# Kernel optimization log

Measured on AMD Instinct MI355X. Metric: run time of the kernel, lower is better.

Reference implementation:

```python
import jax, jax.numpy as jnp
import numpy as np

EPS = 1e-6

def _phi(x):
    # elu(x) + 1 feature map
    return jax.nn.elu(x) + 1.0

def setup_inputs() -> dict:
    key = jax.random.key(0)
    kq, kk, kv = jax.random.split(key, 3)
    N, L, S, H, D, M = 8, 4096, 4096, 8, 64, 64
    queries = jax.random.normal(kq, (N, L, H, D), dtype=jnp.float32)
    keys = jax.random.normal(kk, (N, S, H, D), dtype=jnp.float32)
    values = jax.random.normal(kv, (N, S, H, M), dtype=jnp.float32)
    key_mask = jnp.ones((N, S), dtype=jnp.float32)  # key_lengths.float_matrix
    return {"queries": queries, "keys": keys, "values": values, "key_mask": key_mask}

def reference(queries, keys, values, key_mask):
    Q = _phi(queries)                                   # [N,L,H,D]
    K = _phi(keys) * key_mask[:, :, None, None]         # [N,S,H,D]
    KV = jnp.einsum('nshd,nshm->nhmd', K, values)       # [N,H,M,D]
    Z = 1.0 / (jnp.einsum('nlhd,nhd->nlh', Q, K.sum(axis=1)) + EPS)  # [N,L,H]
    V = jnp.einsum('nlhd,nhmd,nlh->nlhm', Q, KV, Z)     # [N,L,H,M]
    return V
```

## Files before the change

kernel.cpp:

```cpp
#include <hip/hip_runtime.h>


#define SLEN 4096
#define LLEN 4096
#define NHTOT 64
#define HD   512
#define NSPLIT 16
#define EPSF 1e-6f

__device__ __forceinline__ float phi(float x) {
    return x > 0.0f ? x + 1.0f : __expf(x);
}

__device__ __forceinline__ void fma4(float4& a, float s, const float4& b) {
    a.x = fmaf(s, b.x, a.x);
    a.y = fmaf(s, b.y, a.y);
    a.z = fmaf(s, b.z, a.z);
    a.w = fmaf(s, b.w, a.w);
}

__global__ __launch_bounds__(256)
void la_phase1(const float* __restrict__ Kg, const float* __restrict__ Vg,
               const float* __restrict__ maskg,
               float* __restrict__ KVp, float* __restrict__ Ksump) {
    __shared__ float kb[64 * 68];
    __shared__ float vb[64 * 64];
    __shared__ float ksb[16 * 64];

    const int tid  = threadIdx.x;
    const int w    = tid >> 6;
    const int lane = tid & 63;
    const int nh   = blockIdx.y;
    const int n    = nh >> 3;
    const int h    = nh & 7;
    const int sp   = blockIdx.x;

    const int sr = tid >> 4;
    const int c4 = (tid & 15) * 4;
    const int wd = w & 1, wm = w >> 1;
    const int d0 = wd * 32 + (lane & 7) * 4;
    const int m0 = wm * 32 + (lane >> 3) * 4;

    const size_t base = (size_t)n * SLEN * HD + (size_t)h * 64;
    const float* mrow = maskg + (size_t)n * SLEN;
    const int sblock = sp * 256;

    float4 acc[4];
    #pragma unroll
    for (int i = 0; i < 4; ++i) acc[i] = make_float4(0.f, 0.f, 0.f, 0.f);
    float4 ksp = make_float4(0.f, 0.f, 0.f, 0.f);

    for (int t = 0; t < 4; ++t) {
        const int srow0 = sblock + t * 64;
        __syncthreads();
        #pragma unroll
        for (int u = 0; u < 4; ++u) {
            const int row = sr + u * 16;
            const int s   = srow0 + row;
            const size_t g = base + (size_t)s * HD + c4;
            float4 kf = *(const float4*)(Kg + g);
            const float mm = mrow[s];
            kf.x = phi(kf.x) * mm;
            kf.y = phi(kf.y) * mm;
            kf.z = phi(kf.z) * mm;
            kf.w = phi(kf.w) * mm;
            ksp.x += kf.x; ksp.y += kf.y; ksp.z += kf.z; ksp.w += kf.w;
            *(float4*)&kb[row * 68 + c4] = kf;
            *(float4*)&vb[row * 64 + c4] = *(const float4*)(Vg + g);
        }
        __syncthreads();
        #pragma unroll 8
        for (int s = 0; s < 64; ++s) {
            const float4 k4 = *(const float4*)&kb[s * 68 + d0];
            const float4 v4 = *(const float4*)&vb[s * 64 + m0];
            fma4(acc[0], k4.x, v4);
            fma4(acc[1], k4.y, v4);
            fma4(acc[2], k4.z, v4);
            fma4(acc[3], k4.w, v4);
        }
    }

    float* outp = KVp + ((size_t)sp * NHTOT + nh) * 4096;
    #pragma unroll
    for (int di = 0; di < 4; ++di)
        *(float4*)&outp[(d0 + di) * 64 + m0] = acc[di];

    *(float4*)&ksb[sr * 64 + c4] = ksp;
    __syncthreads();
    if (tid < 64) {
        float ssum = 0.f;
        #pragma unroll
        for (int r = 0; r < 16; ++r) ssum += ksb[r * 64 + tid];
        Ksump[((size_t)sp * NHTOT + nh) * 64 + tid] = ssum;
    }
}

__global__ __launch_bounds__(256)
void la_reduce(const float* __restrict__ KVp, const float* __restrict__ Ksump,
               float* __restrict__ KVt, float* __restrict__ Ksum) {
    const int nh  = blockIdx.x;
    const int tid = threadIdx.x;
    #pragma unroll
    for (int j = 0; j < 4; ++j) {
        const int f = (j * 256 + tid) * 4;
        float4 a = make_float4(0.f, 0.f, 0.f, 0.f);
        #pragma unroll
        for (int s = 0; s < NSPLIT; ++s) {
            const float4 v = *(const float4*)&KVp[((size_t)s * NHTOT + nh) * 4096 + f];
            a.x += v.x; a.y += v.y; a.z += v.z; a.w += v.w;
        }
        *(float4*)&KVt[(size_t)nh * 4096 + f] = a;
    }
    if (tid < 64) {
        float a = 0.f;
        #pragma unroll
        for (int s = 0; s < NSPLIT; ++s)
            a += Ksump[((size_t)s * NHTOT + nh) * 64 + tid];
        Ksum[nh * 64 + tid] = a;
    }
}

__global__ __launch_bounds__(256)
void la_phase2(const float* __restrict__ Qg, const float* __restrict__ KVt,
               const float* __restrict__ Ksum, float* __restrict__ Og) {
    __shared__ float Qs[128 * 68];
    __shared__ float KVs[64 * 64];
    __shared__ float KSs[64];

    const int tid = threadIdx.x;
    const int nh  = blockIdx.y;
    const int n   = nh >> 3;
    const int h   = nh & 7;
    const int lbase = blockIdx.x * 128;

    #pragma unroll
    for (int j = 0; j < 4; ++j) {
        const int f = (j * 256 + tid) * 4;
        *(float4*)&KVs[f] = *(const float4*)&KVt[(size_t)nh * 4096 + f];
    }
    if (tid < 16) *(float4*)&KSs[tid * 4] = *(const float4*)&Ksum[nh * 64 + tid * 4];

    const int sr = tid >> 4;
    const int c4 = (tid & 15) * 4;
    #pragma unroll
    for (int u = 0; u < 8; ++u) {
        const int row = sr + u * 16;
        float4 q = *(const float4*)&Qg[((size_t)(n * LLEN + lbase + row) * 8 + h) * 64 + c4];
        q.x = phi(q.x); q.y = phi(q.y); q.z = phi(q.z); q.w = phi(q.w);
        *(float4*)&Qs[row * 68 + c4] = q;
    }
    __syncthreads();

    const int w    = tid >> 6;
    const int lane = tid & 63;
    const int ty   = lane >> 4;
    const int tx   = lane & 15;
    const int m0   = tx * 4;
    const int rb   = w * 32 + ty;

    float4 acc[8];
    float  den[8];
    #pragma unroll
    for (int i = 0; i < 8; ++i) {
        acc[i] = make_float4(0.f, 0.f, 0.f, 0.f);
        den[i] = 0.f;
    }

    for (int d4 = 0; d4 < 16; ++d4) {
        const float4 ks = *(const float4*)&KSs[d4 * 4];
        float4 q4[8];
        #pragma unroll
        for (int i = 0; i < 8; ++i)
            q4[i] = *(const float4*)&Qs[(rb + 4 * i) * 68 + d4 * 4];
        #pragma unroll
        for (int i = 0; i < 8; ++i) {
            den[i] = fmaf(q4[i].x, ks.x, den[i]);
            den[i] = fmaf(q4[i].y, ks.y, den[i]);
            den[i] = fmaf(q4[i].z, ks.z, den[i]);
            den[i] = fmaf(q4[i].w, ks.w, den[i]);
        }
        #pragma unroll
        for (int dk = 0; dk < 4; ++dk) {
            const float4 kv = *(const float4*)&KVs[(d4 * 4 + dk) * 64 + m0];
            #pragma unroll
            for (int i = 0; i < 8; ++i)
                fma4(acc[i], (&q4[i].x)[dk], kv);
        }
    }

    #pragma unroll
    for (int i = 0; i < 8; ++i) {
        const int l = lbase + rb + 4 * i;
        const float z = 1.0f / (den[i] + EPSF);
        float4 o = acc[i];
        o.x *= z; o.y *= z; o.z *= z; o.w *= z;
        *(float4*)&Og[((size_t)(n * LLEN + l) * 8 + h) * 64 + m0] = o;
    }
}

extern "C" void kernel_launch(void* const* d_in, const int* in_sizes, int n_in,
                              void* d_out, int out_size, void* d_ws, size_t ws_size,
                              hipStream_t stream) {
    const float* Q    = (const float*)d_in[0];
    const float* K    = (const float*)d_in[1];
    const float* V    = (const float*)d_in[2];
    const float* mask = (const float*)d_in[3];
    float* out = (float*)d_out;

    float* KVp   = (float*)d_ws;
    float* Ksump = KVp + (size_t)NSPLIT * NHTOT * 4096;
    float* KVt   = Ksump + (size_t)NSPLIT * NHTOT * 64;
    float* Ksum  = KVt + (size_t)NHTOT * 4096;

    dim3 g1(NSPLIT, NHTOT);
    la_phase1<<<g1, 256, 0, stream>>>(K, V, mask, KVp, Ksump);

    la_reduce<<<NHTOT, 256, 0, stream>>>(KVp, Ksump, KVt, Ksum);

    dim3 g2(LLEN / 128, NHTOT);
    la_phase2<<<g2, 256, 0, stream>>>(Q, KVt, Ksum, out);
}
```

Baseline: 253.4 us.

## Give each wave its own KV tile in phase1 and enlarge phase2 row blocks

```diff
diff --git a/kernel.cpp b/kernel.cpp
--- a/kernel.cpp
+++ b/kernel.cpp
@@ -5,7 +5,7 @@
 #define LLEN 4096
 #define NHTOT 64
 #define HD   512
-#define NSPLIT 16
+#define NSPLIT 4
 #define EPSF 1e-6f
 
 __device__ __forceinline__ float phi(float x) {
@@ -23,8 +23,8 @@
 void la_phase1(const float* __restrict__ Kg, const float* __restrict__ Vg,
                const float* __restrict__ maskg,
                float* __restrict__ KVp, float* __restrict__ Ksump) {
-    __shared__ float kb[64 * 68];
-    __shared__ float vb[64 * 64];
+    __shared__ float kb[4][4096];
+    __shared__ float vb[4][4096];
     __shared__ float ksb[16 * 64];
 
     const int tid  = threadIdx.x;
@@ -35,58 +35,83 @@
     const int h    = nh & 7;
     const int sp   = blockIdx.x;
 
-    const int sr = tid >> 4;
-    const int c4 = (tid & 15) * 4;
-    const int wd = w & 1, wm = w >> 1;
-    const int d0 = wd * 32 + (lane & 7) * 4;
-    const int m0 = wm * 32 + (lane >> 3) * 4;
+    const int sr4 = lane >> 4;
+    const int c4  = (lane & 15) * 4;
+    const int d0  = (lane & 7) * 8;
+    const int m0  = (lane >> 3) * 8;
+
+    float* kw = kb[w];
+    float* vw = vb[w];
 
     const size_t base = (size_t)n * SLEN * HD + (size_t)h * 64;
     const float* mrow = maskg + (size_t)n * SLEN;
-    const int sblock = sp * 256;
-
-    float4 acc[4];
-    #pragma unroll
-    for (int i = 0; i < 4; ++i) acc[i] = make_float4(0.f, 0.f, 0.f, 0.f);
+
+    float4 acc[8][2];
+    #pragma unroll
+    for (int i = 0; i < 8; ++i) {
+        acc[i][0] = make_float4(0.f, 0.f, 0.f, 0.f);
+        acc[i][1] = make_float4(0.f, 0.f, 0.f, 0.f);
+    }
     float4 ksp = make_float4(0.f, 0.f, 0.f, 0.f);
 
     for (int t = 0; t < 4; ++t) {
-        const int srow0 = sblock + t * 64;
-        __syncthreads();
-        #pragma unroll
-        for (int u = 0; u < 4; ++u) {
-            const int row = sr + u * 16;
+        const int srow0 = sp * 1024 + t * 256 + w * 64;
+        #pragma unroll
+        for (int u = 0; u < 16; ++u) {
+            const int row = sr4 + u * 4;
             const int s   = srow0 + row;
             const size_t g = base + (size_t)s * HD + c4;
             float4 kf = *(const float4*)(Kg + g);
+            const float4 vf = *(const float4*)(Vg + g);
             const float mm = mrow[s];
             kf.x = phi(kf.x) * mm;
             kf.y = phi(kf.y) * mm;
             kf.z = phi(kf.z) * mm;
             kf.w = phi(kf.w) * mm;
             ksp.x += kf.x; ksp.y += kf.y; ksp.z += kf.z; ksp.w += kf.w;
-            *(float4*)&kb[row * 68 + c4] = kf;
-            *(float4*)&vb[row * 64 + c4] = *(const float4*)(Vg + g);
-        }
-        __syncthreads();
-        #pragma unroll 8
+            *(float4*)&kw[row * 64 + c4] = kf;
+            *(float4*)&vw[row * 64 + c4] = vf;
+        }
+        #pragma unroll 4
         for (int s = 0; s < 64; ++s) {
-            const float4 k4 = *(const float4*)&kb[s * 68 + d0];
-            const float4 v4 = *(const float4*)&vb[s * 64 + m0];
-            fma4(acc[0], k4.x, v4);
-            fma4(acc[1], k4.y, v4);
-            fma4(acc[2], k4.z, v4);
-            fma4(acc[3], k4.w, v4);
-        }
-    }
+            const float4 ka = *(const float4*)&kw[s * 64 + d0];
+            const float4 kz = *(const float4*)&kw[s * 64 + d0 + 4];
+            const float4 va = *(const float4*)&vw[s * 64 + m0];
+            const float4 vz = *(const float4*)&vw[s * 64 + m0 + 4];
+            fma4(acc[0][0], ka.x, va); fma4(acc[0][1], ka.x, vz);
+            fma4(acc[1][0], ka.y, va); fma4(acc[1][1], ka.y, vz);
+            fma4(acc[2][0], ka.z, va); fma4(acc[2][1], ka.z, vz);
+            fma4(acc[3][0], ka.w, va); fma4(acc[3][1], ka.w, vz);
+            fma4(acc[4][0], kz.x, va); fma4(acc[4][1], kz.x, vz);
+            fma4(acc[5][0], kz.y, va); fma4(acc[5][1], kz.y, vz);
+            fma4(acc[6][0], kz.z, va); fma4(acc[6][1], kz.z, vz);
+            fma4(acc[7][0], kz.w, va); fma4(acc[7][1], kz.w, vz);
+        }
+    }
+
+    *(float4*)&ksb[(w * 4 + sr4) * 64 + c4] = ksp;
+
+    #pragma unroll
+    for (int di = 0; di < 8; ++di) {
+        *(float4*)&kw[(d0 + di) * 64 + m0]     = acc[di][0];
+        *(float4*)&kw[(d0 + di) * 64 + m0 + 4] = acc[di][1];
+    }
+    __syncthreads();
 
     float* outp = KVp + ((size_t)sp * NHTOT + nh) * 4096;
     #pragma unroll
-    for (int di = 0; di < 4; ++di)
-        *(float4*)&outp[(d0 + di) * 64 + m0] = acc[di];
-
-    *(float4*)&ksb[sr * 64 + c4] = ksp;
-    __syncthreads();
+    for (int j = 0; j < 4; ++j) {
+        const int f = (j * 256 + tid) * 4;
+        float4 a  = *(const float4*)&kb[0][f];
+        const float4 b1 = *(const float4*)&kb[1][f];
+        const float4 b2 = *(const float4*)&kb[2][f];
+        const float4 b3 = *(const float4*)&kb[3][f];
+        a.x += b1.x + b2.x + b3.x;
+        a.y += b1.y + b2.y + b3.y;
+        a.z += b1.z + b2.z + b3.z;
+        a.w += b1.w + b2.w + b3.w;
+        *(float4*)&outp[f] = a;
+    }
     if (tid < 64) {
         float ssum = 0.f;
         #pragma unroll
@@ -120,10 +145,10 @@
     }
 }
 
-__global__ __launch_bounds__(256)
+__global__ __launch_bounds__(512)
 void la_phase2(const float* __restrict__ Qg, const float* __restrict__ KVt,
                const float* __restrict__ Ksum, float* __restrict__ Og) {
-    __shared__ float Qs[128 * 68];
+    __shared__ float Qs[512 * 68];
     __shared__ float KVs[64 * 64];
     __shared__ float KSs[64];
 
@@ -131,11 +156,11 @@
     const int nh  = blockIdx.y;
     const int n   = nh >> 3;
     const int h   = nh & 7;
-    const int lbase = blockIdx.x * 128;
-
-    #pragma unroll
-    for (int j = 0; j < 4; ++j) {
-        const int f = (j * 256 + tid) * 4;
+    const int lbase = blockIdx.x * 512;
+
+    #pragma unroll
+    for (int j = 0; j < 2; ++j) {
+        const int f = (j * 512 + tid) * 4;
         *(float4*)&KVs[f] = *(const float4*)&KVt[(size_t)nh * 4096 + f];
     }
     if (tid < 16) *(float4*)&KSs[tid * 4] = *(const float4*)&Ksum[nh * 64 + tid * 4];
@@ -143,8 +168,8 @@
     const int sr = tid >> 4;
     const int c4 = (tid & 15) * 4;
     #pragma unroll
-    for (int u = 0; u < 8; ++u) {
-        const int row = sr + u * 16;
+    for (int u = 0; u < 16; ++u) {
+        const int row = sr + u * 32;
         float4 q = *(const float4*)&Qg[((size_t)(n * LLEN + lbase + row) * 8 + h) * 64 + c4];
         q.x = phi(q.x); q.y = phi(q.y); q.z = phi(q.z); q.w = phi(q.w);
         *(float4*)&Qs[row * 68 + c4] = q;
@@ -156,24 +181,24 @@
     const int ty   = lane >> 4;
     const int tx   = lane & 15;
     const int m0   = tx * 4;
-    const int rb   = w * 32 + ty;
-
-    float4 acc[8];
-    float  den[8];
-    #pragma unroll
-    for (int i = 0; i < 8; ++i) {
+    const int rb   = w * 64 + ty;
+
+    float4 acc[16];
+    float  den[16];
+    #pragma unroll
+    for (int i = 0; i < 16; ++i) {
         acc[i] = make_float4(0.f, 0.f, 0.f, 0.f);
         den[i] = 0.f;
     }
 
     for (int d4 = 0; d4 < 16; ++d4) {
         const float4 ks = *(const float4*)&KSs[d4 * 4];
-        float4 q4[8];
-        #pragma unroll
-        for (int i = 0; i < 8; ++i)
+        float4 q4[16];
+        #pragma unroll
+        for (int i = 0; i < 16; ++i)
             q4[i] = *(const float4*)&Qs[(rb + 4 * i) * 68 + d4 * 4];
         #pragma unroll
-        for (int i = 0; i < 8; ++i) {
+        for (int i = 0; i < 16; ++i) {
             den[i] = fmaf(q4[i].x, ks.x, den[i]);
             den[i] = fmaf(q4[i].y, ks.y, den[i]);
             den[i] = fmaf(q4[i].z, ks.z, den[i]);
@@ -183,13 +208,13 @@
         for (int dk = 0; dk < 4; ++dk) {
             const float4 kv = *(const float4*)&KVs[(d4 * 4 + dk) * 64 + m0];
             #pragma unroll
-            for (int i = 0; i < 8; ++i)
+            for (int i = 0; i < 16; ++i)
                 fma4(acc[i], (&q4[i].x)[dk], kv);
         }
     }
 
     #pragma unroll
-    for (int i = 0; i < 8; ++i) {
+    for (int i = 0; i < 16; ++i) {
         const int l = lbase + rb + 4 * i;
         const float z = 1.0f / (den[i] + EPSF);
         float4 o = acc[i];
@@ -217,6 +242,6 @@
 
     la_reduce<<<NHTOT, 256, 0, stream>>>(KVp, Ksump, KVt, Ksum);
 
-    dim3 g2(LLEN / 128, NHTOT);
-    la_phase2<<<g2, 256, 0, stream>>>(Q, KVt, Ksum, out);
-}
+    dim3 g2(LLEN / 512, NHTOT);
+    la_phase2<<<g2, 512, 0, stream>>>(Q, KVt, Ksum, out);
+}
```

New measurement: 274.4 us. 1.08x slower.
